# Kernel optimization log

Measured on AMD Instinct MI355X. Metric: run time of the kernel, lower is better.

## Reference

```python
import jax, jax.numpy as jnp
import numpy as np

B, L, D = 4, 256, 2048
LE, DE = 2048, 1024
H = 16
HD = D // H  # 128
ROPE_BASE = 10000.0


def apply_rope(q):
    # q: [B, H, L, HD]; rotate interleaved pairs along seq axis L (torchtune-style)
    half = HD // 2
    inv_freq = 1.0 / (ROPE_BASE ** (jnp.arange(0, HD, 2, dtype=jnp.float32) / HD))  # [half]
    pos = jnp.arange(L, dtype=jnp.float32)
    ang = pos[:, None] * inv_freq[None, :]           # [L, half]
    cos = jnp.cos(ang)[None, None, :, :]             # [1,1,L,half]
    sin = jnp.sin(ang)[None, None, :, :]
    qr = q.reshape(B, H, L, half, 2)
    q1, q2 = qr[..., 0], qr[..., 1]
    out = jnp.stack([q1 * cos - q2 * sin, q1 * sin + q2 * cos], axis=-1)
    return out.reshape(B, H, L, HD)


def setup_inputs() -> dict:
    key = jax.random.key(0)
    ks = jax.random.split(key, 7)
    s_d = 1.0 / np.sqrt(D)
    s_e = 1.0 / np.sqrt(DE)
    return {
        "x": jax.random.normal(ks[0], (B, L, D), jnp.float32),
        "encoder_inputs": jax.random.normal(ks[1], (B, LE, DE), jnp.float32),
        "Wq": jax.random.normal(ks[2], (D, D), jnp.float32) * s_d,
        "bq": jnp.zeros((D,), jnp.float32),
        "Wk": jax.random.normal(ks[3], (DE, D), jnp.float32) * s_e,
        "bk": jnp.zeros((D,), jnp.float32),
        "Wv": jax.random.normal(ks[4], (DE, D), jnp.float32) * s_e,
        "bv": jnp.zeros((D,), jnp.float32),
        "Wo": jax.random.normal(ks[5], (D, D), jnp.float32) * s_d,
        "bo": jnp.zeros((D,), jnp.float32),
    }


def reference(x, encoder_inputs, Wq, bq, Wk, bk, Wv, bv, Wo, bo):
    q = (x @ Wq + bq).reshape(B, L, H, HD).transpose(0, 2, 1, 3)              # [B,H,L,HD]
    k = (encoder_inputs @ Wk + bk).reshape(B, LE, H, HD).transpose(0, 2, 1, 3)  # [B,H,Le,HD]
    v = (encoder_inputs @ Wv + bv).reshape(B, LE, H, HD).transpose(0, 2, 1, 3)
    q = apply_rope(q)
    scale = 1.0 / jnp.sqrt(jnp.float32(HD))
    scores = jnp.einsum("bhld,bhmd->bhlm", q, k) * scale                      # [B,H,L,Le]
    attn = jax.nn.softmax(scores, axis=-1)
    ctx = jnp.einsum("bhlm,bhmd->bhld", attn, v)                              # [B,H,L,HD]
    ctx = ctx.transpose(0, 2, 1, 3).reshape(B, L, D)
    return ctx @ Wo + bo
```

## Files before the change

### kernel.cpp

```cpp
#include <hip/hip_runtime.h>


#define B_ 4
#define L_ 256
#define D_ 2048
#define LE_ 2048
#define DE_ 1024
#define H_ 16
#define HD_ 128

using f32x4  = __attribute__((ext_vector_type(4))) float;
using bf16x8 = __attribute__((ext_vector_type(8))) short;

__device__ __forceinline__ unsigned short f2bf(float f) {
    union { float f; unsigned int u; } v; v.f = f;
    unsigned int r = v.u + 0x7fffu + ((v.u >> 16) & 1u);
    return (unsigned short)(r >> 16);
}
__device__ __forceinline__ float b2f(unsigned short h) {
    union { unsigned int u; float f; } v; v.u = ((unsigned int)h) << 16;
    return v.f;
}

__device__ __forceinline__ void load_lds16(const void* g, void* l) {
    __builtin_amdgcn_global_load_lds((const __attribute__((address_space(1))) void*)g,
                                     (__attribute__((address_space(3))) void*)l, 16, 0, 0);
}

__global__ void cast_all(const float* __restrict__ x, const float* __restrict__ enc,
                         unsigned short* __restrict__ x_bf, unsigned short* __restrict__ enc_bf) {
    long i = (long)(blockIdx.x * 256 + threadIdx.x) * 4;
    const float* in;
    unsigned short* out;
    if (i < 2097152) { in = x + i; out = x_bf + i; }
    else             { in = enc + (i - 2097152); out = enc_bf + (i - 2097152); }
    float4 v = *(const float4*)in;
    ushort4 o;
    o.x = f2bf(v.x); o.y = f2bf(v.y); o.z = f2bf(v.z); o.w = f2bf(v.w);
    *(ushort4*)out = o;
}

__global__ void transpose_weights(const float* __restrict__ Wq, const float* __restrict__ Wk,
                                  const float* __restrict__ Wv, const float* __restrict__ Wo,
                                  unsigned short* __restrict__ WqT, unsigned short* __restrict__ WkvT,
                                  unsigned short* __restrict__ WoT) {
    __shared__ float t[32][33];
    const float* in;
    unsigned short* out;
    int R;
    const int C = 2048;
    switch (blockIdx.z) {
        case 0:  in = Wq; out = WqT;                R = 2048; break;
        case 1:  in = Wk; out = WkvT;               R = 1024; break;
        case 2:  in = Wv; out = WkvT + 2048 * 1024; R = 1024; break;
        default: in = Wo; out = WoT;                R = 2048; break;
    }
    int r0 = blockIdx.y * 32, c0 = blockIdx.x * 32;
    if (r0 >= R) return;
    int tx = threadIdx.x, ty = threadIdx.y;
    #pragma unroll
    for (int i = 0; i < 32; i += 8) t[ty + i][tx] = in[(long)(r0 + ty + i) * C + c0 + tx];
    __syncthreads();
    #pragma unroll
    for (int i = 0; i < 32; i += 8) out[(long)(c0 + ty + i) * R + r0 + tx] = f2bf(t[tx][ty + i]);
}

__global__ void combine_q_rope(const float* __restrict__ P, const float* __restrict__ bq,
                               unsigned short* __restrict__ Q) {
    int gid = blockIdx.x * 256 + threadIdx.x;
    int p = gid & 63;
    int h = (gid >> 6) & 15;
    int m = gid >> 10;
    int n = h * 128 + 2 * p;
    long i0 = (long)m * 2048 + n;
    float q1 = bq[n], q2 = bq[n + 1];
    #pragma unroll
    for (int pt = 0; pt < 4; pt++) {
        float2 a = *(const float2*)(P + (long)pt * 2097152 + i0);
        q1 += a.x; q2 += a.y;
    }
    int l = m & 255, b = m >> 8;
    float inv = powf(10000.0f, -(float)p * (1.0f / 64.0f));
    float s, c;
    sincosf((float)l * inv, &s, &c);
    const float sc = 0.08838834764831845f;
    long qi = (((long)(b * 16 + h) * 256 + l) << 7) + 2 * p;
    ushort2 o;
    o.x = f2bf((q1 * c - q2 * s) * sc);
    o.y = f2bf((q1 * s + q2 * c) * sc);
    *(ushort2*)(Q + qi) = o;
}

__global__ void combine_pv(const float* __restrict__ P, unsigned short* __restrict__ ctx) {
    int gid = blockIdx.x * 256 + threadIdx.x;
    long e = (long)gid * 4;
    float4 a = *(const float4*)(P + e);
    #pragma unroll
    for (int pt = 1; pt < 4; pt++) {
        float4 b = *(const float4*)(P + (long)pt * 2097152 + e);
        a.x += b.x; a.y += b.y; a.z += b.z; a.w += b.w;
    }
    int bh = (int)(e >> 15);
    int m  = (int)((e >> 7) & 255);
    int d  = (int)(e & 127);
    int bb = bh >> 4, h = bh & 15;
    ushort4 o;
    o.x = f2bf(a.x); o.y = f2bf(a.y); o.z = f2bf(a.z); o.w = f2bf(a.w);
    *(ushort4*)(ctx + ((long)(bb * 256 + m)) * 2048 + h * 128 + d) = o;
}

__global__ void combine_o(const float* __restrict__ P, const float* __restrict__ bo,
                          float* __restrict__ out) {
    int gid = blockIdx.x * 256 + threadIdx.x;
    long e = (long)gid * 4;
    int n = (int)(e & 2047);
    float4 r = *(const float4*)(bo + n);
    #pragma unroll
    for (int pt = 0; pt < 4; pt++) {
        float4 a = *(const float4*)(P + (long)pt * 2097152 + e);
        r.x += a.x; r.y += a.y; r.z += a.z; r.w += a.w;
    }
    *(float4*)(out + e) = r;
}

__launch_bounds__(256)
__global__ void softmax_rows(unsigned short* __restrict__ S) {
    long row = blockIdx.x;
    unsigned short* p = S + row * 2048;
    int t = threadIdx.x, w = t >> 6, lane = t & 63;
    bf16x8 raw = *(const bf16x8*)(p + t * 8);
    float v[8];
    float mx = -1e30f;
    #pragma unroll
    for (int i = 0; i < 8; i++) { v[i] = b2f((unsigned short)raw[i]); mx = fmaxf(mx, v[i]); }
    #pragma unroll
    for (int o = 32; o; o >>= 1) mx = fmaxf(mx, __shfl_xor(mx, o));
    __shared__ float redm[4], reds[4];
    if (lane == 0) redm[w] = mx;
    __syncthreads();
    mx = fmaxf(fmaxf(redm[0], redm[1]), fmaxf(redm[2], redm[3]));
    float sum = 0.f;
    #pragma unroll
    for (int i = 0; i < 8; i++) { v[i] = __expf(v[i] - mx); sum += v[i]; }
    #pragma unroll
    for (int o = 32; o; o >>= 1) sum += __shfl_xor(sum, o);
    if (lane == 0) reds[w] = sum;
    __syncthreads();
    sum = reds[0] + reds[1] + reds[2] + reds[3];
    float r = 1.0f / sum;
    bf16x8 res;
    #pragma unroll
    for (int i = 0; i < 8; i++) res[i] = (short)f2bf(v[i] * r);
    *(bf16x8*)(p + t * 8) = res;
}

template <int EPI>
__launch_bounds__(256)
__global__ void gemm_bt(const unsigned short* __restrict__ A, const unsigned short* __restrict__ Bt,
                        const float* __restrict__ biasA, const float* __restrict__ biasB,
                        void* __restrict__ outA, void* __restrict__ outB,
                        int M, int N, int K, int lda, int ldb,
                        long strideA, long strideB, int zdiv, int nsplit) {
    __shared__ __align__(16) unsigned short smem[16384];
    const int z = blockIdx.z;
    int s = 0, bh = z;
    if constexpr (EPI == 4) { s = z / zdiv; bh = z - s * zdiv; }
    const unsigned short* Ab = A + (long)bh * strideA + (long)s * K;
    const unsigned short* Bb = Bt + (long)bh * strideB + (long)s * K;
    const int m0 = blockIdx.y * 128, n0 = blockIdx.x * 128;
    const int tid = threadIdx.x;
    const int w = tid >> 6, lane = tid & 63;
    const int quad = lane >> 4, l16 = lane & 15;
    const int wr = w >> 1, wc = w & 1;
    const int srow = lane >> 2;
    const int scol = (lane & 3) * 8;

    f32x4 acc[4][4] = {};

    auto stage = [&](int k0, int p) {
        unsigned short* As = smem + p * 8192;
        unsigned short* Bs = As + 4096;
        #pragma unroll
        for (int q = 0; q < 2; q++) {
            int ci = q * 4 + w;
            int row = ci * 16 + srow;
            load_lds16(Ab + (long)(m0 + row) * lda + k0 + scol, (void*)(As + ci * 512));
            load_lds16(Bb + (long)(n0 + row) * ldb + k0 + scol, (void*)(Bs + ci * 512));
        }
    };

    const int nk = K >> 5;
    stage(0, 0);
    for (int i = 0; i < nk; i++) {
        __syncthreads();
        if (i + 1 < nk) stage((i + 1) << 5, (i + 1) & 1);
        const unsigned short* As = smem + (i & 1) * 8192;
        const unsigned short* Bs = As + 4096;
        bf16x8 af[4], bfr[4];
        #pragma unroll
        for (int ii = 0; ii < 4; ii++) {
            int r = wr * 64 + ii * 16 + l16;
            af[ii] = *(const bf16x8*)(As + r * 32 + quad * 8);
        }
        #pragma unroll
        for (int j = 0; j < 4; j++) {
            int r = wc * 64 + j * 16 + l16;
            bfr[j] = *(const bf16x8*)(Bs + r * 32 + quad * 8);
        }
        #pragma unroll
        for (int ii = 0; ii < 4; ii++)
            #pragma unroll
            for (int j = 0; j < 4; j++)
                acc[ii][j] = __builtin_amdgcn_mfma_f32_16x16x32_bf16(af[ii], bfr[j], acc[ii][j], 0, 0, 0);
    }
    __syncthreads();

    if constexpr (EPI == 1) {
        const int b = m0 >> 11;
        const int le0 = m0 & 2047;
        if (n0 < nsplit) {
            const int h = n0 >> 7;
            unsigned short* dst = (unsigned short*)outA + ((((long)(b * 16 + h)) << 11) << 7);
            #pragma unroll
            for (int pp = 0; pp < 2; pp++) {
                if (wr == pp) {
                    #pragma unroll
                    for (int i = 0; i < 4; i++)
                        #pragma unroll
                        for (int j = 0; j < 4; j++)
                            #pragma unroll
                            for (int r = 0; r < 4; r++) {
                                int ml = i * 16 + quad * 4 + r;
                                int n  = wc * 64 + j * 16 + l16;
                                smem[ml * 136 + n] = f2bf(acc[i][j][r] + biasA[n0 + n]);
                            }
                }
                __syncthreads();
                #pragma unroll
                for (int pass = 0; pass < 4; pass++) {
                    int row = pass * 16 + (tid >> 4);
                    int seg = tid & 15;
                    bf16x8 val = *(const bf16x8*)(smem + row * 136 + seg * 8);
                    long le = le0 + pp * 64 + row;
                    *(bf16x8*)(dst + (le << 7) + seg * 8) = val;
                }
                __syncthreads();
            }
        } else {
            const int n0e = n0 - nsplit;
            const int h = n0e >> 7;
            unsigned short* vbase = (unsigned short*)outB + ((long)(b * 16 + h)) * (128 * 2048);
            #pragma unroll
            for (int pp = 0; pp < 2; pp++) {
                if (wr == pp) {
                    #pragma unroll
                    for (int i = 0; i < 4; i++)
                        #pragma unroll
                        for (int j = 0; j < 4; j++) {
                            int d = wc * 64 + j * 16 + l16;
                            float bvd = biasB[n0e + d];
                            #pragma unroll
                            for (int r = 0; r < 4; r++) {
                                int ml = i * 16 + quad * 4 + r;
                                smem[d * 72 + ml] = f2bf(acc[i][j][r] + bvd);
                            }
                        }
                }
                __syncthreads();
                #pragma unroll
                for (int pass = 0; pass < 4; pass++) {
                    int d = pass * 32 + (tid >> 3);
                    int c = tid & 7;
                    bf16x8 val = *(const bf16x8*)(smem + d * 72 + c * 8);
                    *(bf16x8*)(vbase + (long)d * 2048 + le0 + pp * 64 + c * 8) = val;
                }
                __syncthreads();
            }
        }
    } else if constexpr (EPI == 2) {
        #pragma unroll
        for (int pp = 0; pp < 2; pp++) {
            if (wr == pp) {
                #pragma unroll
                for (int i = 0; i < 4; i++)
                    #pragma unroll
                    for (int j = 0; j < 4; j++)
                        #pragma unroll
                        for (int r = 0; r < 4; r++) {
                            int ml = i * 16 + quad * 4 + r;
                            int n  = wc * 64 + j * 16 + l16;
                            smem[ml * 136 + n] = f2bf(acc[i][j][r]);
                        }
            }
            __syncthreads();
            #pragma unroll
            for (int pass = 0; pass < 4; pass++) {
                int row = pass * 16 + (tid >> 4);
                int seg = tid & 15;
                bf16x8 val = *(const bf16x8*)(smem + row * 136 + seg * 8);
                int m = m0 + pp * 64 + row;
                *(bf16x8*)((unsigned short*)outA + (long)z * M * N + (long)m * N + n0 + seg * 8) = val;
            }
            __syncthreads();
        }
    } else {
        float* smf = (float*)smem;
        long zo = ((long)s * zdiv + bh) * (long)M * N;
        #pragma unroll
        for (int q4 = 0; q4 < 4; q4++) {
            if (wr == (q4 >> 1)) {
                #pragma unroll
                for (int ii = 0; ii < 2; ii++) {
                    int i = (q4 & 1) * 2 + ii;
                    #pragma unroll
                    for (int j = 0; j < 4; j++)
                        #pragma unroll
                        for (int r = 0; r < 4; r++) {
                            int ml = ii * 16 + quad * 4 + r;
                            int n  = wc * 64 + j * 16 + l16;
                            smf[ml * 132 + n] = acc[i][j][r];
                        }
                }
            }
            __syncthreads();
            #pragma unroll
            for (int pass = 0; pass < 4; pass++) {
                int row = pass * 8 + (tid >> 5);
                int seg = tid & 31;
                float4 val = *(const float4*)(smf + row * 132 + seg * 4);
                int m = m0 + q4 * 32 + row;
                *(float4*)((float*)outA + zo + (long)m * N + n0 + seg * 4) = val;
            }
            __syncthreads();
        }
    }
}

extern "C" void kernel_launch(void* const* d_in, const int* in_sizes, int n_in,
                              void* d_out, int out_size, void* d_ws, size_t ws_size,
                              hipStream_t stream) {
    const float* x   = (const float*)d_in[0];
    const float* enc = (const float*)d_in[1];
    const float* Wq  = (const float*)d_in[2];
    const float* bq  = (const float*)d_in[3];
    const float* Wk  = (const float*)d_in[4];
    const float* bk  = (const float*)d_in[5];
    const float* Wv  = (const float*)d_in[6];
    const float* bv  = (const float*)d_in[7];
    const float* Wo  = (const float*)d_in[8];
    const float* bo  = (const float*)d_in[9];
    float* out = (float*)d_out;

    char* ws = (char*)d_ws;
    const size_t MB = 1024 * 1024;
    unsigned short* x_bf   = (unsigned short*)(ws + 0 * MB);
    unsigned short* enc_bf = (unsigned short*)(ws + 4 * MB);
    unsigned short* WqT    = (unsigned short*)(ws + 20 * MB);
    unsigned short* WkvT   = (unsigned short*)(ws + 28 * MB);
    unsigned short* K_bf   = (unsigned short*)(ws + 68 * MB);
    unsigned short* WoT    = (unsigned short*)(ws + 100 * MB);
    unsigned short* Q_bf   = (unsigned short*)(ws + 108 * MB);
    unsigned short* Vt     = (unsigned short*)(ws + 112 * MB);
    unsigned short* S_bf   = (unsigned short*)(ws + 0 * MB);
    float*          Pq     = (float*)(ws + 36 * MB);
    float*          Ppv    = (float*)(ws + 68 * MB);
    float*          Po     = (float*)(ws + 0 * MB);
    unsigned short* ctx_bf = (unsigned short*)(ws + 108 * MB);

    cast_all<<<10240, 256, 0, stream>>>(x, enc, x_bf, enc_bf);

    transpose_weights<<<dim3(64, 64, 4), dim3(32, 8), 0, stream>>>(Wq, Wk, Wv, Wo, WqT, WkvT, WoT);

    gemm_bt<4><<<dim3(16, 8, 4), 256, 0, stream>>>(x_bf, WqT, nullptr, nullptr, Pq, nullptr,
                                                   1024, 2048, 512, 2048, 2048, 0, 0, 1, 0);
    combine_q_rope<<<4096, 256, 0, stream>>>(Pq, bq, Q_bf);

    gemm_bt<1><<<dim3(32, 64, 1), 256, 0, stream>>>(enc_bf, WkvT, bk, bv, K_bf, Vt,
                                                    8192, 4096, 1024, 1024, 1024, 0, 0, 1, 2048);

    gemm_bt<2><<<dim3(16, 2, 64), 256, 0, stream>>>(Q_bf, K_bf, nullptr, nullptr, S_bf, nullptr,
                                                    256, 2048, 128, 128, 128,
                                                    256 * 128, 2048 * 128, 1, 0);
    softmax_rows<<<16384, 256, 0, stream>>>(S_bf);

    gemm_bt<4><<<dim3(1, 2, 256), 256, 0, stream>>>(S_bf, Vt, nullptr, nullptr, Ppv, nullptr,
                                                    256, 128, 512, 2048, 2048,
                                                    256 * 2048, 128 * 2048, 64, 0);
    combine_pv<<<2048, 256, 0, stream>>>(Ppv, ctx_bf);

    gemm_bt<4><<<dim3(16, 8, 4), 256, 0, stream>>>(ctx_bf, WoT, nullptr, nullptr, Po, nullptr,
                                                   1024, 2048, 512, 2048, 2048, 0, 0, 1, 0);
    combine_o<<<2048, 256, 0, stream>>>(Po, bo, out);
}
```

Before: 362.9 us.

## Fuse QK^T, softmax and PV into a single flash-attention kernel

Replaces the separate score GEMM, row softmax, split-K PV GEMM and combine kernel with one flash-attention kernel. Each block handles 64 query rows of one head and streams K/V tiles through LDS with an online softmax, so the bf16 score matrix is never materialized. This removes the large score and split-K partial buffers from global memory and cuts several launches. In exchange the K/V loads are not double-buffered and each tile carries several block-wide barriers for the softmax state, which could leave the kernel latency-bound.

New measurement: 384.4 us. 5.9% more time.

```diff
diff --git a/kernel.cpp b/kernel.cpp
--- a/kernel.cpp
+++ b/kernel.cpp
@@ -91,24 +91,6 @@
     *(ushort2*)(Q + qi) = o;
 }
 
-__global__ void combine_pv(const float* __restrict__ P, unsigned short* __restrict__ ctx) {
-    int gid = blockIdx.x * 256 + threadIdx.x;
-    long e = (long)gid * 4;
-    float4 a = *(const float4*)(P + e);
-    #pragma unroll
-    for (int pt = 1; pt < 4; pt++) {
-        float4 b = *(const float4*)(P + (long)pt * 2097152 + e);
-        a.x += b.x; a.y += b.y; a.z += b.z; a.w += b.w;
-    }
-    int bh = (int)(e >> 15);
-    int m  = (int)((e >> 7) & 255);
-    int d  = (int)(e & 127);
-    int bb = bh >> 4, h = bh & 15;
-    ushort4 o;
-    o.x = f2bf(a.x); o.y = f2bf(a.y); o.z = f2bf(a.z); o.w = f2bf(a.w);
-    *(ushort4*)(ctx + ((long)(bb * 256 + m)) * 2048 + h * 128 + d) = o;
-}
-
 __global__ void combine_o(const float* __restrict__ P, const float* __restrict__ bo,
                           float* __restrict__ out) {
     int gid = blockIdx.x * 256 + threadIdx.x;
@@ -124,34 +106,143 @@
 }
 
 __launch_bounds__(256)
-__global__ void softmax_rows(unsigned short* __restrict__ S) {
-    long row = blockIdx.x;
-    unsigned short* p = S + row * 2048;
-    int t = threadIdx.x, w = t >> 6, lane = t & 63;
-    bf16x8 raw = *(const bf16x8*)(p + t * 8);
-    float v[8];
-    float mx = -1e30f;
-    #pragma unroll
-    for (int i = 0; i < 8; i++) { v[i] = b2f((unsigned short)raw[i]); mx = fmaxf(mx, v[i]); }
-    #pragma unroll
-    for (int o = 32; o; o >>= 1) mx = fmaxf(mx, __shfl_xor(mx, o));
-    __shared__ float redm[4], reds[4];
-    if (lane == 0) redm[w] = mx;
+__global__ void flash_attn(const unsigned short* __restrict__ Q,
+                           const unsigned short* __restrict__ Kb,
+                           const unsigned short* __restrict__ Vtg,
+                           unsigned short* __restrict__ ctx) {
+    __shared__ __align__(16) unsigned short Ks[16384];
+    __shared__ __align__(16) unsigned short Vs[16384];
+    __shared__ __align__(16) unsigned short Ps[64 * 136];
+    __shared__ float m_state[64], l_state[64], nmw[64], alw[64];
+    __shared__ float pmax[64][2], psum[64][2];
+
+    const int bh = blockIdx.y, l0 = blockIdx.x * 64;
+    const int b = bh >> 4, h = bh & 15;
+    const int tid = threadIdx.x, w = tid >> 6, lane = tid & 63;
+    const int quad = lane >> 4, l16 = lane & 15;
+    const int wr = w >> 1, wc = w & 1;
+
+    const unsigned short* Qb = Q   + (((long)bh * 256 + l0) << 7);
+    const unsigned short* Kt = Kb  + ((long)bh << 18);
+    const unsigned short* Vb = Vtg + ((long)bh << 18);
+
+    bf16x8 af[2][4];
+    #pragma unroll
+    for (int i = 0; i < 2; i++)
+        #pragma unroll
+        for (int kk = 0; kk < 4; kk++)
+            af[i][kk] = *(const bf16x8*)(Qb + (long)(wr * 32 + i * 16 + l16) * 128 + kk * 32 + quad * 8);
+
+    f32x4 o[2][4] = {};
+    if (tid < 64) { m_state[tid] = -1e30f; l_state[tid] = 0.f; }
     __syncthreads();
-    mx = fmaxf(fmaxf(redm[0], redm[1]), fmaxf(redm[2], redm[3]));
-    float sum = 0.f;
-    #pragma unroll
-    for (int i = 0; i < 8; i++) { v[i] = __expf(v[i] - mx); sum += v[i]; }
-    #pragma unroll
-    for (int o = 32; o; o >>= 1) sum += __shfl_xor(sum, o);
-    if (lane == 0) reds[w] = sum;
+
+    for (int t = 0; t < 16; t++) {
+        const unsigned short* Kg = Kt + (long)t * 16384;
+        #pragma unroll
+        for (int q = 0; q < 8; q++) {
+            int c = w * 8 + q;
+            load_lds16(Kg + c * 512 + lane * 8, (void*)(Ks + c * 512));
+        }
+        #pragma unroll
+        for (int q = 0; q < 8; q++) {
+            int c = w * 8 + q;
+            int rd = c * 4 + (lane >> 4);
+            load_lds16(Vb + (long)rd * 2048 + t * 128 + (lane & 15) * 8, (void*)(Vs + c * 512));
+        }
+        __syncthreads();
+
+        f32x4 s[2][4] = {};
+        #pragma unroll
+        for (int kk = 0; kk < 4; kk++) {
+            bf16x8 bk[4];
+            #pragma unroll
+            for (int j = 0; j < 4; j++)
+                bk[j] = *(const bf16x8*)(Ks + (wc * 64 + j * 16 + l16) * 128 + kk * 32 + quad * 8);
+            #pragma unroll
+            for (int i = 0; i < 2; i++)
+                #pragma unroll
+                for (int j = 0; j < 4; j++)
+                    s[i][j] = __builtin_amdgcn_mfma_f32_16x16x32_bf16(af[i][kk], bk[j], s[i][j], 0, 0, 0);
+        }
+
+        #pragma unroll
+        for (int i = 0; i < 2; i++)
+            #pragma unroll
+            for (int r = 0; r < 4; r++) {
+                float mx = fmaxf(fmaxf(s[0 + i][0][r], s[i][1][r]), fmaxf(s[i][2][r], s[i][3][r]));
+                #pragma unroll
+                for (int off = 1; off < 16; off <<= 1) mx = fmaxf(mx, __shfl_xor(mx, off));
+                if (l16 == 0) pmax[wr * 32 + i * 16 + quad * 4 + r][wc] = mx;
+            }
+        __syncthreads();
+        if (tid < 64) {
+            float nm = fmaxf(m_state[tid], fmaxf(pmax[tid][0], pmax[tid][1]));
+            alw[tid] = __expf(m_state[tid] - nm);
+            nmw[tid] = nm;
+            m_state[tid] = nm;
+        }
+        __syncthreads();
+
+        #pragma unroll
+        for (int i = 0; i < 2; i++)
+            #pragma unroll
+            for (int r = 0; r < 4; r++) {
+                int row = wr * 32 + i * 16 + quad * 4 + r;
+                float nm = nmw[row];
+                float al = alw[row];
+                float ls = 0.f;
+                #pragma unroll
+                for (int j = 0; j < 4; j++) {
+                    float p = __expf(s[i][j][r] - nm);
+                    s[i][j][r] = p;
+                    ls += p;
+                    o[i][j][r] *= al;
+                    Ps[row * 136 + wc * 64 + j * 16 + l16] = f2bf(p);
+                }
+                #pragma unroll
+                for (int off = 1; off < 16; off <<= 1) ls += __shfl_xor(ls, off);
+                if (l16 == 0) psum[row][wc] = ls;
+            }
+        __syncthreads();
+        if (tid < 64) l_state[tid] = l_state[tid] * alw[tid] + psum[tid][0] + psum[tid][1];
+
+        #pragma unroll
+        for (int kk = 0; kk < 4; kk++) {
+            bf16x8 pa[2], vb[4];
+            #pragma unroll
+            for (int i = 0; i < 2; i++)
+                pa[i] = *(const bf16x8*)(Ps + (wr * 32 + i * 16 + l16) * 136 + kk * 32 + quad * 8);
+            #pragma unroll
+            for (int j = 0; j < 4; j++)
+                vb[j] = *(const bf16x8*)(Vs + (wc * 64 + j * 16 + l16) * 128 + kk * 32 + quad * 8);
+            #pragma unroll
+            for (int i = 0; i < 2; i++)
+                #pragma unroll
+                for (int j = 0; j < 4; j++)
+                    o[i][j] = __builtin_amdgcn_mfma_f32_16x16x32_bf16(pa[i], vb[j], o[i][j], 0, 0, 0);
+        }
+        __syncthreads();
+    }
+
+    #pragma unroll
+    for (int i = 0; i < 2; i++)
+        #pragma unroll
+        for (int r = 0; r < 4; r++) {
+            int row = wr * 32 + i * 16 + quad * 4 + r;
+            float rinv = 1.0f / l_state[row];
+            #pragma unroll
+            for (int j = 0; j < 4; j++)
+                Ps[row * 136 + wc * 64 + j * 16 + l16] = f2bf(o[i][j][r] * rinv);
+        }
     __syncthreads();
-    sum = reds[0] + reds[1] + reds[2] + reds[3];
-    float r = 1.0f / sum;
-    bf16x8 res;
-    #pragma unroll
-    for (int i = 0; i < 8; i++) res[i] = (short)f2bf(v[i] * r);
-    *(bf16x8*)(p + t * 8) = res;
+    #pragma unroll
+    for (int pass = 0; pass < 4; pass++) {
+        int sid = pass * 256 + tid;
+        int row = sid >> 4, seg = sid & 15;
+        bf16x8 val = *(const bf16x8*)(Ps + row * 136 + seg * 8);
+        *(bf16x8*)(ctx + ((long)(b * 256 + l0 + row)) * 2048 + h * 128 + seg * 8) = val;
+    }
 }
 
 template <int EPI>
@@ -277,32 +368,6 @@
                 __syncthreads();
             }
         }
-    } else if constexpr (EPI == 2) {
-        #pragma unroll
-        for (int pp = 0; pp < 2; pp++) {
-            if (wr == pp) {
-                #pragma unroll
-                for (int i = 0; i < 4; i++)
-                    #pragma unroll
-                    for (int j = 0; j < 4; j++)
-                        #pragma unroll
-                        for (int r = 0; r < 4; r++) {
-                            int ml = i * 16 + quad * 4 + r;
-                            int n  = wc * 64 + j * 16 + l16;
-                            smem[ml * 136 + n] = f2bf(acc[i][j][r]);
-                        }
-            }
-            __syncthreads();
-            #pragma unroll
-            for (int pass = 0; pass < 4; pass++) {
-                int row = pass * 16 + (tid >> 4);
-                int seg = tid & 15;
-                bf16x8 val = *(const bf16x8*)(smem + row * 136 + seg * 8);
-                int m = m0 + pp * 64 + row;
-                *(bf16x8*)((unsigned short*)outA + (long)z * M * N + (long)m * N + n0 + seg * 8) = val;
-            }
-            __syncthreads();
-        }
     } else {
         float* smf = (float*)smem;
         long zo = ((long)s * zdiv + bh) * (long)M * N;
@@ -361,11 +426,9 @@
     unsigned short* WoT    = (unsigned short*)(ws + 100 * MB);
     unsigned short* Q_bf   = (unsigned short*)(ws + 108 * MB);
     unsigned short* Vt     = (unsigned short*)(ws + 112 * MB);
-    unsigned short* S_bf   = (unsigned short*)(ws + 0 * MB);
     float*          Pq     = (float*)(ws + 36 * MB);
-    float*          Ppv    = (float*)(ws + 68 * MB);
-    float*          Po     = (float*)(ws + 0 * MB);
-    unsigned short* ctx_bf = (unsigned short*)(ws + 108 * MB);
+    unsigned short* ctx_bf = (unsigned short*)(ws + 0 * MB);
+    float*          Po     = (float*)(ws + 8 * MB);
 
     cast_all<<<10240, 256, 0, stream>>>(x, enc, x_bf, enc_bf);
 
@@ -378,15 +441,7 @@
     gemm_bt<1><<<dim3(32, 64, 1), 256, 0, stream>>>(enc_bf, WkvT, bk, bv, K_bf, Vt,
                                                     8192, 4096, 1024, 1024, 1024, 0, 0, 1, 2048);
 
-    gemm_bt<2><<<dim3(16, 2, 64), 256, 0, stream>>>(Q_bf, K_bf, nullptr, nullptr, S_bf, nullptr,
-                                                    256, 2048, 128, 128, 128,
-                                                    256 * 128, 2048 * 128, 1, 0);
-    softmax_rows<<<16384, 256, 0, stream>>>(S_bf);
-
-    gemm_bt<4><<<dim3(1, 2, 256), 256, 0, stream>>>(S_bf, Vt, nullptr, nullptr, Ppv, nullptr,
-                                                    256, 128, 512, 2048, 2048,
-                                                    256 * 2048, 128 * 2048, 64, 0);
-    combine_pv<<<2048, 256, 0, stream>>>(Ppv, ctx_bf);
+    flash_attn<<<dim3(4, 64), 256, 0, stream>>>(Q_bf, K_bf, Vt, ctx_bf);
 
     gemm_bt<4><<<dim3(16, 8, 4), 256, 0, stream>>>(ctx_bf, WoT, nullptr, nullptr, Po, nullptr,
                                                    1024, 2048, 512, 2048, 2048, 0, 0, 1, 0);
```
